# Performance work log

Measured on AMD Instinct MI355X. Metric: run time of the kernel, lower is better.

## Reference

```python
import jax, jax.numpy as jnp
import numpy as np

N_HEAD = 16
D_K = 64
D_MODEL = N_HEAD * D_K
LN_EPS = 1e-5


def setup_inputs() -> dict:
    key = jax.random.key(0)
    ks = jax.random.split(key, 11)
    B, Tq, Tk = 4, 2048, 2048
    s = 1.0 / np.sqrt(D_MODEL)
    return {
        "q": jax.random.normal(ks[0], (B, Tq, D_MODEL), jnp.float32),
        "k": jax.random.normal(ks[1], (B, Tk, D_MODEL), jnp.float32),
        "v": jax.random.normal(ks[2], (B, Tk, D_MODEL), jnp.float32),
        "Wq": jax.random.normal(ks[3], (D_MODEL, D_MODEL), jnp.float32) * s,
        "bq": jnp.zeros((D_MODEL,), jnp.float32),
        "Wk": jax.random.normal(ks[4], (D_MODEL, D_MODEL), jnp.float32) * s,
        "bk": jnp.zeros((D_MODEL,), jnp.float32),
        "Wv": jax.random.normal(ks[5], (D_MODEL, D_MODEL), jnp.float32) * s,
        "bv": jnp.zeros((D_MODEL,), jnp.float32),
        "Wo": jax.random.normal(ks[6], (D_MODEL, D_MODEL), jnp.float32) * s,
        "bo": jnp.zeros((D_MODEL,), jnp.float32),
        "gamma": jnp.ones((D_MODEL,), jnp.float32),
        "beta": jnp.zeros((D_MODEL,), jnp.float32),
    }


def reference(q, k, v, Wq, bq, Wk, bk, Wv, bv, Wo, bo, gamma, beta):
    B, Tq, _ = q.shape
    Tk = k.shape[1]
    temperature = jnp.asarray(D_K ** 0.5, q.dtype)

    # projections (torch Linear: x @ W.T + b), reshape to heads: [B, T, H, DK]
    qh = (q @ Wq.T + bq).reshape(B, Tq, N_HEAD, D_K)
    kh = (k @ Wk.T + bk).reshape(B, Tk, N_HEAD, D_K)
    vh = (v @ Wv.T + bv).reshape(B, Tk, N_HEAD, D_K)

    # scores [B, H, Tq, Tk]; softmax over Tk (dropout is identity in eval)
    scores = jnp.einsum('bqhd,bkhd->bhqk', qh, kh) / temperature
    attn = jax.nn.softmax(scores, axis=-1)

    # attention output -> concat heads [B, Tq, D_MODEL]
    out = jnp.einsum('bhqk,bkhd->bqhd', attn, vh).reshape(B, Tq, D_MODEL)

    out = out @ Wo.T + bo
    x = out + q  # residual
    mu = jnp.mean(x, axis=-1, keepdims=True)
    var = jnp.var(x, axis=-1, keepdims=True)
    out_norm = (x - mu) * jax.lax.rsqrt(var + LN_EPS) * gamma + beta

    # attn returned in torch layout [NHead*B, Tq, Tk]
    attn_flat = attn.transpose(1, 0, 2, 3).reshape(N_HEAD * B, Tq, Tk)
    return (out_norm, attn_flat)
```

## Files before the change

### kernel.cpp

```cpp
#include <hip/hip_runtime.h>
#include <cstdint>
#include <cstddef>

typedef __attribute__((ext_vector_type(4))) float f32x4;
typedef __attribute__((ext_vector_type(8))) short s16x8;
typedef __attribute__((ext_vector_type(8))) _Float16 f16x8;
typedef __attribute__((ext_vector_type(4))) unsigned short u16x4;
typedef __attribute__((ext_vector_type(8))) unsigned short u16x8;

#define MFMA_BF16(a, b, c) __builtin_amdgcn_mfma_f32_16x16x32_bf16((a), (b), (c), 0, 0, 0)
#define MFMA_F16(a, b, c) __builtin_amdgcn_mfma_f32_16x16x32_f16((a), (b), (c), 0, 0, 0)
#define GLOAD_LDS16(src, dst)                                             \
  __builtin_amdgcn_global_load_lds(                                       \
      (const __attribute__((address_space(1))) void*)(src),               \
      (__attribute__((address_space(3))) void*)(dst), 16, 0, 0)

static constexpr int kD = 1024;
static constexpr int kT = 2048;

__device__ __forceinline__ unsigned short f2bf(float f) {
  union { float f; uint32_t u; } v; v.f = f;
  uint32_t r = v.u + 0x7fffu + ((v.u >> 16) & 1u);
  return (unsigned short)(r >> 16);
}
__device__ __forceinline__ unsigned short f2h(float f) {
  union { _Float16 h; unsigned short u; } cv;
  cv.h = (_Float16)f;
  return cv.u;
}

__global__ __launch_bounds__(256) void convert_all_k(
    const float* __restrict__ q, const float* __restrict__ k,
    const float* __restrict__ v, const float* __restrict__ Wq,
    const float* __restrict__ Wk, const float* __restrict__ Wv,
    const float* __restrict__ Wo, unsigned short* __restrict__ q_h,
    unsigned short* __restrict__ k_h, unsigned short* __restrict__ v_b,
    unsigned short* __restrict__ Wq_h, unsigned short* __restrict__ Wk_h,
    unsigned short* __restrict__ Wv_b, unsigned short* __restrict__ Wo_b) {
  constexpr int nq4 = (4 * 2048 * 1024) / 4;
  constexpr int nw4 = (1024 * 1024) / 4;
  constexpr int total = 3 * nq4 + 4 * nw4;
  for (int i = blockIdx.x * 256 + threadIdx.x; i < total; i += gridDim.x * 256) {
    const float* src;
    unsigned short* dst;
    int off;
    bool use_f16;
    if (i < nq4) { src = q; dst = q_h; off = i; use_f16 = true; }
    else if (i < 2 * nq4) { src = k; dst = k_h; off = i - nq4; use_f16 = true; }
    else if (i < 3 * nq4) { src = v; dst = v_b; off = i - 2 * nq4; use_f16 = false; }
    else if (i < 3 * nq4 + nw4) { src = Wq; dst = Wq_h; off = i - 3 * nq4; use_f16 = true; }
    else if (i < 3 * nq4 + 2 * nw4) { src = Wk; dst = Wk_h; off = i - 3 * nq4 - nw4; use_f16 = true; }
    else if (i < 3 * nq4 + 3 * nw4) { src = Wv; dst = Wv_b; off = i - 3 * nq4 - 2 * nw4; use_f16 = false; }
    else { src = Wo; dst = Wo_b; off = i - 3 * nq4 - 3 * nw4; use_f16 = false; }
    f32x4 vv = ((const f32x4*)src)[off];
    u16x4 o4;
#pragma unroll
    for (int j = 0; j < 4; j++) o4[j] = use_f16 ? f2h(vv[j]) : f2bf(vv[j]);
    ((u16x4*)dst)[off] = o4;
  }
}

template <int MODE>
__global__ __launch_bounds__(256, 3) void gemm_16(
    const unsigned short* __restrict__ X, const unsigned short* __restrict__ W,
    const float* __restrict__ bias, const float* __restrict__ resid,
    unsigned short* __restrict__ outB, float* __restrict__ outF, float oscale) {
  __shared__ unsigned short smem[2 * 128 * 64];
  unsigned short* Ah = smem;
  unsigned short* Bh = smem + 8192;

  const int tid = threadIdx.x, lane = tid & 63, w = tid >> 6;
  const int wg = (blockIdx.x & 7) * 64 + (blockIdx.x >> 3);
  const int m0 = (wg >> 3) * 128, n0 = (wg & 7) * 128;
  const int wm0 = (w >> 1) * 64, wn0 = (w & 1) * 64;
  const int lr = lane & 15, lk = lane >> 4;
  const int srow = lane >> 3, sslot = (lane & 7) ^ srow;

  const size_t xoff = (size_t)(m0 + w * 32 + srow) * kD + sslot * 8;
  const size_t woff = (size_t)(n0 + w * 32 + srow) * kD + sslot * 8;

  f32x4 acc[4][4];
#pragma unroll
  for (int i = 0; i < 4; i++)
#pragma unroll
    for (int j = 0; j < 4; j++) acc[i][j] = (f32x4){0.f, 0.f, 0.f, 0.f};

  for (int kt = 0; kt < kD / 64; ++kt) {
    __syncthreads();
    const int kof = kt * 64;
#pragma unroll
    for (int i = 0; i < 4; i++) {
      const int ldst = (w * 32 + i * 8) * 64;
      GLOAD_LDS16(X + xoff + (size_t)i * 8 * kD + kof, &Ah[ldst]);
      GLOAD_LDS16(W + woff + (size_t)i * 8 * kD + kof, &Bh[ldst]);
    }
    __syncthreads();
#pragma unroll
    for (int ks = 0; ks < 2; ks++) {
      s16x8 af[4], bf[4];
#pragma unroll
      for (int i = 0; i < 4; i++) {
        const int ra = wm0 + i * 16 + lr;
        const int oa = ra * 128 + ((((ks * 4) + lk) ^ (ra & 7)) << 4);
        const int rb = wn0 + i * 16 + lr;
        const int ob = rb * 128 + ((((ks * 4) + lk) ^ (rb & 7)) << 4);
        af[i] = *(const s16x8*)((const char*)Ah + oa);
        bf[i] = *(const s16x8*)((const char*)Bh + ob);
      }
#pragma unroll
      for (int i = 0; i < 4; i++)
#pragma unroll
        for (int j = 0; j < 4; j++) {
          if constexpr (MODE == 0) {
            acc[i][j] = MFMA_F16(*(const f16x8*)&af[i], *(const f16x8*)&bf[j],
                                 acc[i][j]);
          } else {
            acc[i][j] = MFMA_BF16(af[i], bf[j], acc[i][j]);
          }
        }
    }
  }

#pragma unroll
  for (int j = 0; j < 4; j++) {
    const int col = n0 + wn0 + j * 16 + lr;
    const float bv = bias[col];
#pragma unroll
    for (int i = 0; i < 4; i++)
#pragma unroll
      for (int r = 0; r < 4; r++) {
        const int row = m0 + wm0 + i * 16 + lk * 4 + r;
        const size_t idx = (size_t)row * kD + col;
        float vv = acc[i][j][r] + bv;
        if constexpr (MODE == 0) {
          outB[idx] = f2h(vv * oscale);
        } else if constexpr (MODE == 1) {
          outB[idx] = f2bf(vv);
        } else {
          outF[idx] = vv + resid[idx];
        }
      }
  }
}

__global__ __launch_bounds__(256) void transpose_v(
    const unsigned short* __restrict__ vh, unsigned short* __restrict__ vhT) {
  __shared__ unsigned short lds[64 * 72];
  const int bx = blockIdx.x;
  const int tt = bx & 31, bhp = bx >> 5;
  const int b = bhp >> 4, h = bhp & 15;
  const int t0 = tt * 64, tid = threadIdx.x;
  {
    const int t = tid >> 2, c0 = (tid & 3) * 16;
    const unsigned short* src = &vh[(size_t)(b * kT + t0 + t) * kD + h * 64 + c0];
    u16x8 v0 = *(const u16x8*)src;
    u16x8 v1 = *(const u16x8*)(src + 8);
    *(u16x8*)&lds[t * 72 + c0] = v0;
    *(u16x8*)&lds[t * 72 + c0 + 8] = v1;
  }
  __syncthreads();
  {
    const int d = tid >> 2, tc0 = (tid & 3) * 16;
    u16x8 o0, o1;
#pragma unroll
    for (int i = 0; i < 8; i++) o0[i] = lds[(tc0 + i) * 72 + d];
#pragma unroll
    for (int i = 0; i < 8; i++) o1[i] = lds[(tc0 + 8 + i) * 72 + d];
    size_t base = ((size_t)((b * 16 + h) * 64 + d)) * kT + t0 + tc0;
    *(u16x8*)&vhT[base] = o0;
    *(u16x8*)&vhT[base + 8] = o1;
  }
}

__global__ __launch_bounds__(256, 3) void attn_fused(
    const unsigned short* __restrict__ qh, const unsigned short* __restrict__ kh,
    const unsigned short* __restrict__ vhT, unsigned short* __restrict__ attn_out,
    float* __restrict__ attn_p) {
  __shared__ unsigned short kbuf[2][64 * 64];
  __shared__ unsigned short vbuf[2][64 * 64];
  __shared__ unsigned short qp[9216];

  const int tid = threadIdx.x, lane = tid & 63, w = tid >> 6;
  const int lr = lane & 15, lk = lane >> 4;
  const int srow = lane >> 3, sslot = (lane & 7) ^ srow;
  const int wg = (blockIdx.x & 7) * 128 + (blockIdx.x >> 3);
  const int bh = wg >> 4, qt = wg & 15;
  const int h = bh >> 2, b = bh & 3;
  const int q0 = qt * 128, qm0 = w * 32;

  const size_t qsrc = (size_t)(b * kT + q0 + w * 32 + srow) * kD + h * 64 + sslot * 8;
#pragma unroll
  for (int i = 0; i < 4; i++)
    GLOAD_LDS16(qh + qsrc + (size_t)i * 8 * kD, &qp[(w * 32 + i * 8) * 64]);

  const size_t kbase = (size_t)(b * kT + w * 16 + srow) * kD + h * 64 + sslot * 8;
  const size_t vbase = ((size_t)((b * 16 + h) * 64) + w * 16 + srow) * kT + sslot * 8;

#pragma unroll
  for (int i = 0; i < 2; i++)
    GLOAD_LDS16(kh + kbase + (size_t)(i * 8) * kD, &kbuf[0][(w * 16 + i * 8) * 64]);
  __syncthreads();

  f16x8 qf[2][2];
#pragma unroll
  for (int mq = 0; mq < 2; mq++)
#pragma unroll
    for (int ks = 0; ks < 2; ks++) {
      const int rq = qm0 + mq * 16 + lr;
      qf[mq][ks] = *(const f16x8*)((const char*)qp + rq * 128 +
                                   ((((ks * 4) + lk) ^ (rq & 7)) << 4));
    }

  float l_part[2] = {0.f, 0.f};

  for (int kt = 0; kt < kT / 64; ++kt) {
    if (kt + 1 < kT / 64) {
#pragma unroll
      for (int i = 0; i < 2; i++)
        GLOAD_LDS16(kh + kbase + (size_t)((kt + 1) * 64 + i * 8) * kD,
                    &kbuf[(kt + 1) & 1][(w * 16 + i * 8) * 64]);
    }
    const unsigned short* kb = kbuf[kt & 1];
    f32x4 sc[2][4];
#pragma unroll
    for (int mq = 0; mq < 2; mq++)
#pragma unroll
      for (int ni = 0; ni < 4; ni++) sc[mq][ni] = (f32x4){0.f, 0.f, 0.f, 0.f};
#pragma unroll
    for (int ks = 0; ks < 2; ks++) {
      f16x8 kf[4];
#pragma unroll
      for (int ni = 0; ni < 4; ni++) {
        const int rk = ni * 16 + lr;
        kf[ni] = *(const f16x8*)((const char*)kb + rk * 128 +
                                 ((((ks * 4) + lk) ^ (rk & 7)) << 4));
      }
#pragma unroll
      for (int mq = 0; mq < 2; mq++)
#pragma unroll
        for (int ni = 0; ni < 4; ni++)
          sc[mq][ni] = MFMA_F16(kf[ni], qf[mq][ks], sc[mq][ni]);
    }
#pragma unroll
    for (int mq = 0; mq < 2; mq++)
#pragma unroll
      for (int ni = 0; ni < 4; ni++)
        l_part[mq] += __expf(sc[mq][ni][0]) + __expf(sc[mq][ni][1]) +
                      __expf(sc[mq][ni][2]) + __expf(sc[mq][ni][3]);
    __syncthreads();
  }

  float rl[2];
#pragma unroll
  for (int mq = 0; mq < 2; mq++) {
    float s = l_part[mq];
    s += __shfl_xor(s, 16, 64);
    s += __shfl_xor(s, 32, 64);
    rl[mq] = 1.0f / s;
  }

  f32x4 pv[2][4];
#pragma unroll
  for (int mq = 0; mq < 2; mq++)
#pragma unroll
    for (int nd = 0; nd < 4; nd++) pv[mq][nd] = (f32x4){0.f, 0.f, 0.f, 0.f};

#pragma unroll
  for (int i = 0; i < 2; i++) {
    const int ldst = (w * 16 + i * 8) * 64;
    GLOAD_LDS16(kh + kbase + (size_t)(i * 8) * kD, &kbuf[0][ldst]);
    GLOAD_LDS16(vhT + vbase + (size_t)i * 8 * kT, &vbuf[0][ldst]);
  }
  unsigned short* p_w = &qp[w * 2304];
  __syncthreads();

  for (int kt = 0; kt < kT / 64; ++kt) {
    if (kt + 1 < kT / 64) {
#pragma unroll
      for (int i = 0; i < 2; i++) {
        const int ldst = (w * 16 + i * 8) * 64;
        GLOAD_LDS16(kh + kbase + (size_t)((kt + 1) * 64 + i * 8) * kD,
                    &kbuf[(kt + 1) & 1][ldst]);
        GLOAD_LDS16(vhT + vbase + (size_t)i * 8 * kT + (kt + 1) * 64,
                    &vbuf[(kt + 1) & 1][ldst]);
      }
    }
    const unsigned short* kb = kbuf[kt & 1];
    const unsigned short* vb = vbuf[kt & 1];
    f32x4 sc[2][4];
#pragma unroll
    for (int mq = 0; mq < 2; mq++)
#pragma unroll
      for (int ni = 0; ni < 4; ni++) sc[mq][ni] = (f32x4){0.f, 0.f, 0.f, 0.f};
#pragma unroll
    for (int ks = 0; ks < 2; ks++) {
      f16x8 kf[4];
#pragma unroll
      for (int ni = 0; ni < 4; ni++) {
        const int rk = ni * 16 + lr;
        kf[ni] = *(const f16x8*)((const char*)kb + rk * 128 +
                                 ((((ks * 4) + lk) ^ (rk & 7)) << 4));
      }
#pragma unroll
      for (int mq = 0; mq < 2; mq++)
#pragma unroll
        for (int ni = 0; ni < 4; ni++)
          sc[mq][ni] = MFMA_F16(kf[ni], qf[mq][ks], sc[mq][ni]);
    }
#pragma unroll
    for (int mq = 0; mq < 2; mq++) {
      const int qrow = q0 + qm0 + mq * 16 + lr;
      float* prow = attn_p + ((size_t)(bh * kT + qrow)) * kT + kt * 64 + 4 * lk;
#pragma unroll
      for (int ni = 0; ni < 4; ni++) {
        f32x4 pr;
#pragma unroll
        for (int r = 0; r < 4; r++) pr[r] = __expf(sc[mq][ni][r]) * rl[mq];
        __builtin_nontemporal_store(pr, (f32x4*)(prow + ni * 16));
        uint32_t d0, d1;
        asm("v_cvt_pk_bf16_f32 %0, %1, %2" : "=v"(d0) : "v"(pr[0]), "v"(pr[1]));
        asm("v_cvt_pk_bf16_f32 %0, %1, %2" : "=v"(d1) : "v"(pr[2]), "v"(pr[3]));
        uint2 dd; dd.x = d0; dd.y = d1;
        *(uint2*)&p_w[(mq * 16 + lr) * 72 + ni * 16 + 4 * lk] = dd;
      }
    }
#pragma unroll
    for (int ks = 0; ks < 2; ks++) {
      s16x8 pf[2], vf[4];
#pragma unroll
      for (int mq = 0; mq < 2; mq++)
        pf[mq] = *(const s16x8*)&p_w[(mq * 16 + lr) * 72 + ks * 32 + lk * 8];
#pragma unroll
      for (int nd = 0; nd < 4; nd++) {
        const int row = nd * 16 + lr;
        const int sw2 = ((ks * 4) + lk) ^ (row & 7);
        vf[nd] = *(const s16x8*)((const char*)vb + row * 128 + (sw2 << 4));
      }
#pragma unroll
      for (int mq = 0; mq < 2; mq++)
#pragma unroll
        for (int nd = 0; nd < 4; nd++)
          pv[mq][nd] = MFMA_BF16(pf[mq], vf[nd], pv[mq][nd]);
    }
    __syncthreads();
  }

#pragma unroll
  for (int mq = 0; mq < 2; mq++)
#pragma unroll
    for (int nd = 0; nd < 4; nd++)
#pragma unroll
      for (int r = 0; r < 4; r++) {
        const int qrow = q0 + qm0 + mq * 16 + lk * 4 + r;
        attn_out[((size_t)(b * kT + qrow)) * kD + h * 64 + nd * 16 + lr] =
            f2bf(pv[mq][nd][r]);
      }
}

__global__ __launch_bounds__(256) void ln_kernel(
    const float* __restrict__ x, const float* __restrict__ gamma,
    const float* __restrict__ beta, float* __restrict__ out) {
  __shared__ float ssum[4], ssq[4];
  const int row = blockIdx.x, tid = threadIdx.x;
  f32x4 v = *(const f32x4*)&x[(size_t)row * kD + tid * 4];
  float s = v[0] + v[1] + v[2] + v[3];
  float q2 = v[0] * v[0] + v[1] * v[1] + v[2] * v[2] + v[3] * v[3];
#pragma unroll
  for (int d = 1; d < 64; d <<= 1) {
    s += __shfl_xor(s, d, 64);
    q2 += __shfl_xor(q2, d, 64);
  }
  const int w = tid >> 6, lane = tid & 63;
  if (lane == 0) {
    ssum[w] = s;
    ssq[w] = q2;
  }
  __syncthreads();
  s = ssum[0] + ssum[1] + ssum[2] + ssum[3];
  q2 = ssq[0] + ssq[1] + ssq[2] + ssq[3];
  const float mu = s * (1.f / 1024.f);
  const float var = q2 * (1.f / 1024.f) - mu * mu;
  const float rstd = rsqrtf(var + 1e-5f);
  f32x4 g = *(const f32x4*)&gamma[tid * 4];
  f32x4 bb = *(const f32x4*)&beta[tid * 4];
  f32x4 o;
#pragma unroll
  for (int j = 0; j < 4; j++) o[j] = (v[j] - mu) * rstd * g[j] + bb[j];
  *(f32x4*)&out[(size_t)row * kD + tid * 4] = o;
}

extern "C" void kernel_launch(void* const* d_in, const int* in_sizes, int n_in,
                              void* d_out, int out_size, void* d_ws,
                              size_t ws_size, hipStream_t stream) {
  const float* q = (const float*)d_in[0];
  const float* k = (const float*)d_in[1];
  const float* v = (const float*)d_in[2];
  const float* Wq = (const float*)d_in[3];
  const float* bq = (const float*)d_in[4];
  const float* Wk = (const float*)d_in[5];
  const float* bk = (const float*)d_in[6];
  const float* Wv = (const float*)d_in[7];
  const float* bv = (const float*)d_in[8];
  const float* Wo = (const float*)d_in[9];
  const float* bo = (const float*)d_in[10];
  const float* gamma = (const float*)d_in[11];
  const float* beta = (const float*)d_in[12];

  float* out = (float*)d_out;
  float* attn_p = out + (size_t)8192 * 1024;

  constexpr size_t NQ = (size_t)4 * 2048 * 1024;
  constexpr size_t NW = (size_t)1024 * 1024;

  unsigned short* w16 = (unsigned short*)d_ws;
  unsigned short* q_h  = w16 + 0 * NQ;
  unsigned short* k_h  = w16 + 1 * NQ;
  unsigned short* v_b  = w16 + 2 * NQ;
  unsigned short* qh_h = w16 + 3 * NQ;
  unsigned short* kh_h = w16 + 4 * NQ;
  unsigned short* vh_b = w16 + 5 * NQ;
  unsigned short* vhT  = w16 + 6 * NQ;
  unsigned short* ao_b = w16 + 7 * NQ;
  unsigned short* Wq_h = w16 + 8 * NQ;
  unsigned short* Wk_h = Wq_h + NW;
  unsigned short* Wv_b = Wq_h + 2 * NW;
  unsigned short* Wo_b = Wq_h + 3 * NW;
  float* xbuf = (float*)(Wq_h + 4 * NW);

  dim3 blk(256);
  convert_all_k<<<2048, blk, 0, stream>>>(q, k, v, Wq, Wk, Wv, Wo, q_h, k_h,
                                          v_b, Wq_h, Wk_h, Wv_b, Wo_b);

  gemm_16<0><<<512, blk, 0, stream>>>(q_h, Wq_h, bq, nullptr, qh_h, nullptr,
                                      0.125f);
  gemm_16<0><<<512, blk, 0, stream>>>(k_h, Wk_h, bk, nullptr, kh_h, nullptr,
                                      1.0f);
  gemm_16<1><<<512, blk, 0, stream>>>(v_b, Wv_b, bv, nullptr, vh_b, nullptr,
                                      1.0f);
  transpose_v<<<2048, blk, 0, stream>>>(vh_b, vhT);
  attn_fused<<<1024, blk, 0, stream>>>(qh_h, kh_h, vhT, ao_b, attn_p);
  gemm_16<2><<<512, blk, 0, stream>>>(ao_b, Wo_b, bo, q, nullptr, xbuf, 1.0f);
  ln_kernel<<<8192, blk, 0, stream>>>(xbuf, gamma, beta, out);
}
```

Baseline: 506.2 us.

## Fuse V transpose into V GEMM epilogue and reorder attention passes

The V projection GEMM now writes its output already transposed per head, staging each tile through shared memory, so the separate transpose kernel and its extra global round trip are gone. The attention kernel now runs the P·V pass first with unnormalized exponentials and applies the row-sum reciprocal to the output at the end. A second QK pass then writes the normalized probabilities. This reorder was probably meant to make the two passes share setup, but each pass still recomputes QK^T. The reorder also leaves the unnormalized bf16 probabilities without scaling, which could overflow if scores are large.

```diff
diff --git a/kernel.cpp b/kernel.cpp
--- a/kernel.cpp
+++ b/kernel.cpp
@@ -65,7 +65,7 @@
     const unsigned short* __restrict__ X, const unsigned short* __restrict__ W,
     const float* __restrict__ bias, const float* __restrict__ resid,
     unsigned short* __restrict__ outB, float* __restrict__ outF, float oscale) {
-  __shared__ unsigned short smem[2 * 128 * 64];
+  __shared__ unsigned short smem[MODE == 1 ? 16640 : 16384];
   unsigned short* Ah = smem;
   unsigned short* Bh = smem + 8192;
 
@@ -121,6 +121,33 @@
     }
   }
 
+  if constexpr (MODE == 1) {
+    __syncthreads();
+#pragma unroll
+    for (int j = 0; j < 4; j++) {
+      const int col = wn0 + j * 16 + lr;
+      const float bv = bias[n0 + col];
+#pragma unroll
+      for (int i = 0; i < 4; i++)
+#pragma unroll
+        for (int r = 0; r < 4; r++) {
+          const int row = wm0 + i * 16 + lk * 4 + r;
+          smem[col * 130 + row] = f2bf(acc[i][j][r] + bv);
+        }
+    }
+    __syncthreads();
+    const int b = m0 >> 11, t0 = m0 & 2047;
+    const int dl = tid >> 1, th = (tid & 1) * 64;
+    const int h = (n0 + dl) >> 6, dh = (n0 + dl) & 63;
+    unsigned short* dst = outB + ((size_t)((b * 16 + h) * 64 + dh)) * kT + t0 + th;
+#pragma unroll
+    for (int i = 0; i < 8; i++) {
+      u16x8 o = *(const u16x8*)&smem[dl * 130 + th + i * 8];
+      *(u16x8*)(dst + i * 8) = o;
+    }
+    return;
+  }
+
 #pragma unroll
   for (int j = 0; j < 4; j++) {
     const int col = n0 + wn0 + j * 16 + lr;
@@ -134,41 +161,10 @@
         float vv = acc[i][j][r] + bv;
         if constexpr (MODE == 0) {
           outB[idx] = f2h(vv * oscale);
-        } else if constexpr (MODE == 1) {
-          outB[idx] = f2bf(vv);
         } else {
           outF[idx] = vv + resid[idx];
         }
       }
-  }
-}
-
-__global__ __launch_bounds__(256) void transpose_v(
-    const unsigned short* __restrict__ vh, unsigned short* __restrict__ vhT) {
-  __shared__ unsigned short lds[64 * 72];
-  const int bx = blockIdx.x;
-  const int tt = bx & 31, bhp = bx >> 5;
-  const int b = bhp >> 4, h = bhp & 15;
-  const int t0 = tt * 64, tid = threadIdx.x;
-  {
-    const int t = tid >> 2, c0 = (tid & 3) * 16;
-    const unsigned short* src = &vh[(size_t)(b * kT + t0 + t) * kD + h * 64 + c0];
-    u16x8 v0 = *(const u16x8*)src;
-    u16x8 v1 = *(const u16x8*)(src + 8);
-    *(u16x8*)&lds[t * 72 + c0] = v0;
-    *(u16x8*)&lds[t * 72 + c0 + 8] = v1;
-  }
-  __syncthreads();
-  {
-    const int d = tid >> 2, tc0 = (tid & 3) * 16;
-    u16x8 o0, o1;
-#pragma unroll
-    for (int i = 0; i < 8; i++) o0[i] = lds[(tc0 + i) * 72 + d];
-#pragma unroll
-    for (int i = 0; i < 8; i++) o1[i] = lds[(tc0 + 8 + i) * 72 + d];
-    size_t base = ((size_t)((b * 16 + h) * 64 + d)) * kT + t0 + tc0;
-    *(u16x8*)&vhT[base] = o0;
-    *(u16x8*)&vhT[base + 8] = o1;
   }
 }
 
@@ -197,8 +193,11 @@
   const size_t vbase = ((size_t)((b * 16 + h) * 64) + w * 16 + srow) * kT + sslot * 8;
 
 #pragma unroll
-  for (int i = 0; i < 2; i++)
-    GLOAD_LDS16(kh + kbase + (size_t)(i * 8) * kD, &kbuf[0][(w * 16 + i * 8) * 64]);
+  for (int i = 0; i < 2; i++) {
+    const int ldst = (w * 16 + i * 8) * 64;
+    GLOAD_LDS16(kh + kbase + (size_t)(i * 8) * kD, &kbuf[0][ldst]);
+    GLOAD_LDS16(vhT + vbase + (size_t)i * 8 * kT, &vbuf[0][ldst]);
+  }
   __syncthreads();
 
   f16x8 qf[2][2];
@@ -212,67 +211,12 @@
     }
 
   float l_part[2] = {0.f, 0.f};
-
-  for (int kt = 0; kt < kT / 64; ++kt) {
-    if (kt + 1 < kT / 64) {
-#pragma unroll
-      for (int i = 0; i < 2; i++)
-        GLOAD_LDS16(kh + kbase + (size_t)((kt + 1) * 64 + i * 8) * kD,
-                    &kbuf[(kt + 1) & 1][(w * 16 + i * 8) * 64]);
-    }
-    const unsigned short* kb = kbuf[kt & 1];
-    f32x4 sc[2][4];
-#pragma unroll
-    for (int mq = 0; mq < 2; mq++)
-#pragma unroll
-      for (int ni = 0; ni < 4; ni++) sc[mq][ni] = (f32x4){0.f, 0.f, 0.f, 0.f};
-#pragma unroll
-    for (int ks = 0; ks < 2; ks++) {
-      f16x8 kf[4];
-#pragma unroll
-      for (int ni = 0; ni < 4; ni++) {
-        const int rk = ni * 16 + lr;
-        kf[ni] = *(const f16x8*)((const char*)kb + rk * 128 +
-                                 ((((ks * 4) + lk) ^ (rk & 7)) << 4));
-      }
-#pragma unroll
-      for (int mq = 0; mq < 2; mq++)
-#pragma unroll
-        for (int ni = 0; ni < 4; ni++)
-          sc[mq][ni] = MFMA_F16(kf[ni], qf[mq][ks], sc[mq][ni]);
-    }
-#pragma unroll
-    for (int mq = 0; mq < 2; mq++)
-#pragma unroll
-      for (int ni = 0; ni < 4; ni++)
-        l_part[mq] += __expf(sc[mq][ni][0]) + __expf(sc[mq][ni][1]) +
-                      __expf(sc[mq][ni][2]) + __expf(sc[mq][ni][3]);
-    __syncthreads();
-  }
-
-  float rl[2];
-#pragma unroll
-  for (int mq = 0; mq < 2; mq++) {
-    float s = l_part[mq];
-    s += __shfl_xor(s, 16, 64);
-    s += __shfl_xor(s, 32, 64);
-    rl[mq] = 1.0f / s;
-  }
-
   f32x4 pv[2][4];
 #pragma unroll
   for (int mq = 0; mq < 2; mq++)
 #pragma unroll
     for (int nd = 0; nd < 4; nd++) pv[mq][nd] = (f32x4){0.f, 0.f, 0.f, 0.f};
-
-#pragma unroll
-  for (int i = 0; i < 2; i++) {
-    const int ldst = (w * 16 + i * 8) * 64;
-    GLOAD_LDS16(kh + kbase + (size_t)(i * 8) * kD, &kbuf[0][ldst]);
-    GLOAD_LDS16(vhT + vbase + (size_t)i * 8 * kT, &vbuf[0][ldst]);
-  }
   unsigned short* p_w = &qp[w * 2304];
-  __syncthreads();
 
   for (int kt = 0; kt < kT / 64; ++kt) {
     if (kt + 1 < kT / 64) {
@@ -309,14 +253,12 @@
     }
 #pragma unroll
     for (int mq = 0; mq < 2; mq++) {
-      const int qrow = q0 + qm0 + mq * 16 + lr;
-      float* prow = attn_p + ((size_t)(bh * kT + qrow)) * kT + kt * 64 + 4 * lk;
 #pragma unroll
       for (int ni = 0; ni < 4; ni++) {
         f32x4 pr;
 #pragma unroll
-        for (int r = 0; r < 4; r++) pr[r] = __expf(sc[mq][ni][r]) * rl[mq];
-        __builtin_nontemporal_store(pr, (f32x4*)(prow + ni * 16));
+        for (int r = 0; r < 4; r++) pr[r] = __expf(sc[mq][ni][r]);
+        l_part[mq] += pr[0] + pr[1] + pr[2] + pr[3];
         uint32_t d0, d1;
         asm("v_cvt_pk_bf16_f32 %0, %1, %2" : "=v"(d0) : "v"(pr[0]), "v"(pr[1]));
         asm("v_cvt_pk_bf16_f32 %0, %1, %2" : "=v"(d1) : "v"(pr[2]), "v"(pr[3]));
@@ -345,16 +287,75 @@
     __syncthreads();
   }
 
+  float rl[2];
+#pragma unroll
+  for (int mq = 0; mq < 2; mq++) {
+    float s = l_part[mq];
+    s += __shfl_xor(s, 16, 64);
+    s += __shfl_xor(s, 32, 64);
+    rl[mq] = 1.0f / s;
+  }
 #pragma unroll
   for (int mq = 0; mq < 2; mq++)
 #pragma unroll
-    for (int nd = 0; nd < 4; nd++)
-#pragma unroll
-      for (int r = 0; r < 4; r++) {
-        const int qrow = q0 + qm0 + mq * 16 + lk * 4 + r;
+    for (int r = 0; r < 4; r++) {
+      const int qloc = lk * 4 + r;
+      const float rlq = __shfl(rl[mq], qloc, 64);
+#pragma unroll
+      for (int nd = 0; nd < 4; nd++) {
+        const int qrow = q0 + qm0 + mq * 16 + qloc;
         attn_out[((size_t)(b * kT + qrow)) * kD + h * 64 + nd * 16 + lr] =
-            f2bf(pv[mq][nd][r]);
-      }
+            f2bf(pv[mq][nd][r] * rlq);
+      }
+    }
+
+#pragma unroll
+  for (int i = 0; i < 2; i++)
+    GLOAD_LDS16(kh + kbase + (size_t)(i * 8) * kD, &kbuf[0][(w * 16 + i * 8) * 64]);
+  __syncthreads();
+
+  for (int kt = 0; kt < kT / 64; ++kt) {
+    if (kt + 1 < kT / 64) {
+#pragma unroll
+      for (int i = 0; i < 2; i++)
+        GLOAD_LDS16(kh + kbase + (size_t)((kt + 1) * 64 + i * 8) * kD,
+                    &kbuf[(kt + 1) & 1][(w * 16 + i * 8) * 64]);
+    }
+    const unsigned short* kb = kbuf[kt & 1];
+    f32x4 sc[2][4];
+#pragma unroll
+    for (int mq = 0; mq < 2; mq++)
+#pragma unroll
+      for (int ni = 0; ni < 4; ni++) sc[mq][ni] = (f32x4){0.f, 0.f, 0.f, 0.f};
+#pragma unroll
+    for (int ks = 0; ks < 2; ks++) {
+      f16x8 kf[4];
+#pragma unroll
+      for (int ni = 0; ni < 4; ni++) {
+        const int rk = ni * 16 + lr;
+        kf[ni] = *(const f16x8*)((const char*)kb + rk * 128 +
+                                 ((((ks * 4) + lk) ^ (rk & 7)) << 4));
+      }
+#pragma unroll
+      for (int mq = 0; mq < 2; mq++)
+#pragma unroll
+        for (int ni = 0; ni < 4; ni++)
+          sc[mq][ni] = MFMA_F16(kf[ni], qf[mq][ks], sc[mq][ni]);
+    }
+#pragma unroll
+    for (int mq = 0; mq < 2; mq++) {
+      const int qrow = q0 + qm0 + mq * 16 + lr;
+      float* prow = attn_p + ((size_t)(bh * kT + qrow)) * kT + kt * 64 + 4 * lk;
+#pragma unroll
+      for (int ni = 0; ni < 4; ni++) {
+        f32x4 pr;
+#pragma unroll
+        for (int r = 0; r < 4; r++) pr[r] = __expf(sc[mq][ni][r]) * rl[mq];
+        __builtin_nontemporal_store(pr, (f32x4*)(prow + ni * 16));
+      }
+    }
+    __syncthreads();
+  }
 }
 
 __global__ __launch_bounds__(256) void ln_kernel(
@@ -418,10 +419,9 @@
   unsigned short* v_b  = w16 + 2 * NQ;
   unsigned short* qh_h = w16 + 3 * NQ;
   unsigned short* kh_h = w16 + 4 * NQ;
-  unsigned short* vh_b = w16 + 5 * NQ;
-  unsigned short* vhT  = w16 + 6 * NQ;
-  unsigned short* ao_b = w16 + 7 * NQ;
-  unsigned short* Wq_h = w16 + 8 * NQ;
+  unsigned short* vhT  = w16 + 5 * NQ;
+  unsigned short* ao_b = w16 + 6 * NQ;
+  unsigned short* Wq_h = w16 + 7 * NQ;
   unsigned short* Wk_h = Wq_h + NW;
   unsigned short* Wv_b = Wq_h + 2 * NW;
   unsigned short* Wo_b = Wq_h + 3 * NW;
@@ -435,9 +435,8 @@
                                       0.125f);
   gemm_16<0><<<512, blk, 0, stream>>>(k_h, Wk_h, bk, nullptr, kh_h, nullptr,
                                       1.0f);
-  gemm_16<1><<<512, blk, 0, stream>>>(v_b, Wv_b, bv, nullptr, vh_b, nullptr,
+  gemm_16<1><<<512, blk, 0, stream>>>(v_b, Wv_b, bv, nullptr, vhT, nullptr,
                                       1.0f);
-  transpose_v<<<2048, blk, 0, stream>>>(vh_b, vhT);
   attn_fused<<<1024, blk, 0, stream>>>(qh_h, kh_h, vhT, ao_b, attn_p);
   gemm_16<2><<<512, blk, 0, stream>>>(ao_b, Wo_b, bo, q, nullptr, xbuf, 1.0f);
   ln_kernel<<<8192, blk, 0, stream>>>(xbuf, gamma, beta, out);
```

New measurement: 509.4 us, median of 3. Within noise of the previous version (+0.6%).
